# Kernel optimization log

Hardware: AMD Instinct MI355X
Metric: run time of the kernel (lower is better)

Reference implementation:

```python
import jax, jax.numpy as jnp
import numpy as np

T = 2048        # q_len (current chunk)
P = 2048        # past KV cache length
HID = 4096      # hidden_size
H = 32          # num_attention_heads
D = HID // H    # head_dim = 128
THETA = 10000.0


def apply_rope(x, pos):
    # x: [H, T, D], pos: [T] int
    half = D // 2
    inv_freq = 1.0 / (THETA ** (jnp.arange(0, half, dtype=jnp.float32) / half))
    ang = pos.astype(jnp.float32)[:, None] * inv_freq[None, :]      # [T, D/2]
    cos = jnp.concatenate([jnp.cos(ang), jnp.cos(ang)], axis=-1)[None]  # [1, T, D]
    sin = jnp.concatenate([jnp.sin(ang), jnp.sin(ang)], axis=-1)[None]
    rot = jnp.concatenate([-x[..., half:], x[..., :half]], axis=-1)
    return x * cos + rot * sin


def setup_inputs() -> dict:
    key = jax.random.key(0)
    ks = jax.random.split(key, 8)
    s = 1.0 / np.sqrt(HID)
    inp = {
        "hidden_states": jax.random.normal(ks[0], (T, HID), dtype=jnp.float32),
        "attention_mask": jnp.triu(jnp.full((T, T), -jnp.inf, dtype=jnp.float32), k=1),
        "Wq": jax.random.normal(ks[1], (HID, HID), dtype=jnp.float32) * s,
        "Wk": jax.random.normal(ks[2], (HID, HID), dtype=jnp.float32) * s,
        "Wv": jax.random.normal(ks[3], (HID, HID), dtype=jnp.float32) * s,
        "Wo": jax.random.normal(ks[4], (HID, HID), dtype=jnp.float32) * s,
        "past_k": jax.random.normal(ks[5], (H, P, D), dtype=jnp.float32),
        "past_v": jax.random.normal(ks[6], (H, P, D), dtype=jnp.float32),
        "position_ids": P + jnp.arange(T, dtype=jnp.int32),
        "past_length": P,
    }
    return inp


def reference(hidden_states, attention_mask, Wq, Wk, Wv, Wo, past_k, past_v,
              position_ids, past_length):
    # QKV projections -> [H, T, D]
    proj = lambda W: (hidden_states @ W).reshape(T, H, D).transpose(1, 0, 2)
    q, k, v = proj(Wq), proj(Wk), proj(Wv)
    q = apply_rope(q, position_ids)
    k = apply_rope(k, position_ids)

    scale = 1.0 / jnp.sqrt(jnp.float32(D))
    # scores against past cache and current chunk (fp32 softmax, as in source)
    past_dots = (jnp.einsum('htd,hsd->hts', q, past_k) * scale).astype(jnp.float32)
    pmask = jnp.where(jnp.arange(P) < past_length, 0.0, -jnp.inf)  # [P]
    past_dots = past_dots + pmask
    cur = ((jnp.einsum('htd,hsd->hts', q, k) * scale) + attention_mask).astype(jnp.float32)

    # online-softmax merge via logsumexp combination
    past_lse = jax.scipy.special.logsumexp(past_dots, axis=-1, keepdims=True)
    cur_lse = jax.scipy.special.logsumexp(cur, axis=-1, keepdims=True)
    tot_lse = jnp.logaddexp(past_lse, cur_lse)
    pw = jnp.exp(past_dots - tot_lse).astype(q.dtype)
    cw = jnp.exp(cur - tot_lse).astype(q.dtype)

    out = jnp.einsum('hts,hsd->htd', pw, past_v) + jnp.einsum('hts,hsd->htd', cw, v)
    out = jnp.where(past_length == 0,
                    jnp.einsum('hts,hsd->htd', jax.nn.softmax(cur, axis=-1).astype(q.dtype), v),
                    out)
    out = out.transpose(1, 0, 2).reshape(T, HID)   # [T, hidden]
    return out @ Wo
```

## Files before the change

kernel.cpp:

```cpp
#include <hip/hip_runtime.h>
#include <cstdint>
#include <cstddef>

#define T_LEN 2048
#define PAST_MAX 2048
#define HID 4096
#define NHEAD 32
#define DHEAD 128

typedef __bf16 bf16_t;
typedef __bf16 bf16x4 __attribute__((ext_vector_type(4)));
typedef __bf16 bf16x8 __attribute__((ext_vector_type(8)));
typedef float  f32x4  __attribute__((ext_vector_type(4)));
typedef float  f32x16 __attribute__((ext_vector_type(16)));
typedef unsigned int u32x4 __attribute__((ext_vector_type(4)));

__device__ __forceinline__ void gload16(const void* g, void* l){
  __builtin_amdgcn_global_load_lds((const __attribute__((address_space(1))) void*)g,
                                   (__attribute__((address_space(3))) void*)l,
                                   16, 0, 0);
}

__device__ __forceinline__ unsigned pack_bf16(float a, float b){
  const unsigned ua = __builtin_bit_cast(unsigned short, (bf16_t)a);
  const unsigned ub = __builtin_bit_cast(unsigned short, (bf16_t)b);
  return ua | (ub << 16);
}

__global__ void cvt2_k(const float* __restrict__ a, bf16_t* __restrict__ ao,
                       const float* __restrict__ b, bf16_t* __restrict__ bo, int n4){
  int i = blockIdx.x * 256 + threadIdx.x;
  if (i < n4){
    const float4 v = ((const float4*)a)[i];
    bf16x4 o = { (bf16_t)v.x, (bf16_t)v.y, (bf16_t)v.z, (bf16_t)v.w };
    ((bf16x4*)ao)[i] = o;
  } else {
    i -= n4;
    const float4 v = ((const float4*)b)[i];
    bf16x4 o = { (bf16_t)v.x, (bf16_t)v.y, (bf16_t)v.z, (bf16_t)v.w };
    ((bf16x4*)bo)[i] = o;
  }
}

__global__ __launch_bounds__(256) void transpose2_k(const float* __restrict__ in,
                                                    bf16_t* __restrict__ out, int R, int C){
  __shared__ float tile[64][65];
  const int r0 = blockIdx.x << 6, c0 = blockIdx.y << 6;
  const size_t bo = (size_t)blockIdx.z * (size_t)R * (size_t)C;
  const int tx = threadIdx.x & 15, ty = threadIdx.x >> 4;
#pragma unroll
  for (int k = 0; k < 4; ++k){
    const float4 v = *(const float4*)(in + bo + (size_t)(r0 + ty + 16*k) * C + c0 + tx*4);
    float* tp = &tile[ty + 16*k][tx*4];
    tp[0] = v.x; tp[1] = v.y; tp[2] = v.z; tp[3] = v.w;
  }
  __syncthreads();
  const int rr0 = (threadIdx.x & 7) * 8;
  const int ccb = threadIdx.x >> 3;
#pragma unroll
  for (int k = 0; k < 2; ++k){
    const int cc = ccb + 32*k;
    bf16x8 o;
#pragma unroll
    for (int j = 0; j < 8; ++j) o[j] = (bf16_t)tile[rr0 + j][cc];
    *(bf16x8*)(out + bo + (size_t)(c0 + cc) * R + r0 + rr0) = o;
  }
}

__global__ __launch_bounds__(256) void transpose3_k(
    const float* __restrict__ s0, const float* __restrict__ s1, const float* __restrict__ s2,
    bf16_t* __restrict__ d0, bf16_t* __restrict__ d1, bf16_t* __restrict__ d2){
  __shared__ float tile[64][65];
  const float* in = (blockIdx.z == 0) ? s0 : (blockIdx.z == 1) ? s1 : s2;
  bf16_t* out = (blockIdx.z == 0) ? d0 : (blockIdx.z == 1) ? d1 : d2;
  const int r0 = blockIdx.x << 6, c0 = blockIdx.y << 6;
  const int tx = threadIdx.x & 15, ty = threadIdx.x >> 4;
#pragma unroll
  for (int k = 0; k < 4; ++k){
    const float4 v = *(const float4*)(in + (size_t)(r0 + ty + 16*k) * HID + c0 + tx*4);
    float* tp = &tile[ty + 16*k][tx*4];
    tp[0] = v.x; tp[1] = v.y; tp[2] = v.z; tp[3] = v.w;
  }
  __syncthreads();
  const int rr0 = (threadIdx.x & 7) * 8;
  const int ccb = threadIdx.x >> 3;
#pragma unroll
  for (int k = 0; k < 2; ++k){
    const int cc = ccb + 32*k;
    bf16x8 o;
#pragma unroll
    for (int j = 0; j < 8; ++j) o[j] = (bf16_t)tile[rr0 + j][cc];
    *(bf16x8*)(out + (size_t)(c0 + cc) * HID + r0 + rr0) = o;
  }
}

__global__ void ropek_k(bf16_t* __restrict__ K, const int* __restrict__ pos){
  const int idx = blockIdx.x * 256 + threadIdx.x;
  const int i = idx & 63;
  const int t = (idx >> 6) & (T_LEN - 1);
  const int h = idx >> 17;
  const size_t base = ((size_t)h * T_LEN + t) * DHEAD;
  const float p = (float)pos[t];
  const float inv = __expf(-(float)i * 0.14391156605212898f);
  const float ang = p * inv;
  float sn, cs;
  sincosf(ang, &sn, &cs);
  const float b0 = (float)K[base + i], b1 = (float)K[base + i + 64];
  K[base + i]      = (bf16_t)(b0 * cs - b1 * sn);
  K[base + i + 64] = (bf16_t)(b1 * cs + b0 * sn);
}

__global__ __launch_bounds__(512, 2) void gemm2b_k(
    const bf16_t* __restrict__ A,
    const bf16_t* __restrict__ B0, const bf16_t* __restrict__ B1, const bf16_t* __restrict__ B2,
    bf16_t* __restrict__ OQ, bf16_t* __restrict__ OK2, bf16_t* __restrict__ OVT, int cpx)
{
  const int bid = blockIdx.x;
  const int wg  = (bid & 7) * cpx + (bid >> 3);
  const int mt  = wg & 7;
  const int rest = wg >> 3;
  const int z   = rest >> 5;
  const int nt  = rest & 31;
  const int m0  = mt << 8;
  const int n0  = nt << 7;
  const bf16_t* __restrict__ B = (z == 0) ? B0 : (z == 1) ? B1 : B2;

  const int tid = threadIdx.x;
  const int wv = tid >> 6, lane = tid & 63, lm = lane & 15, g = lane >> 4;
  const int wr = wv >> 1, wc = wv & 1;

  __shared__ __align__(16) char smem[49152];

  const f32x4 fzero = {0.f, 0.f, 0.f, 0.f};
  f32x4 acc[4][4];
#pragma unroll
  for (int i = 0; i < 4; ++i)
#pragma unroll
    for (int j = 0; j < 4; ++j) acc[i][j] = fzero;

  size_t aoff[2], boff;
#pragma unroll
  for (int i = 0; i < 2; ++i){
    const int c = i * 512 + tid;
    const int row = c >> 2, gr = c & 3;
    const int srcg = gr ^ ((row >> 1) & 3);
    aoff[i] = (size_t)(m0 + row) * HID + srcg * 8;
  }
  {
    const int row = tid >> 2, gr = tid & 3;
    const int srcg = gr ^ ((row >> 1) & 3);
    boff = (size_t)(n0 + row) * HID + srcg * 8;
  }
  const int adst0 = ((0 * 512 + wv * 64) << 4);
  const int adst1 = ((1 * 512 + wv * 64) << 4);
  const int bdst  = ((wv * 64) << 4);

  auto stage = [&](int kt){
    char* ab = smem + (kt & 1) * 24576;
    char* bb = ab + 16384;
    const bf16_t* Ak = A + kt * 32;
    const bf16_t* Bk = B + kt * 32;
    gload16(Ak + aoff[0], ab + adst0);
    gload16(Ak + aoff[1], ab + adst1);
    gload16(Bk + boff,    bb + bdst);
  };

  const int ksw = ((g ^ ((lm >> 1) & 3)) << 4);
  const int arow = (wr * 64 + lm) * 64;
  const int brow = (wc * 64 + lm) * 64;

  const int NT = HID / 32;
  stage(0);
  for (int t = 0; t < NT; ++t){
    if (t + 1 < NT){
      stage(t + 1);
      asm volatile("s_waitcnt vmcnt(3)" ::: "memory");
    } else {
      asm volatile("s_waitcnt vmcnt(0)" ::: "memory");
    }
    __builtin_amdgcn_s_barrier();

    char* ab = smem + (t & 1) * 24576;
    char* bb = ab + 16384;
    bf16x8 af[4], bfv[4];
#pragma unroll
    for (int mf = 0; mf < 4; ++mf)
      af[mf] = *(const bf16x8*)(ab + arow + mf * 1024 + ksw);
#pragma unroll
    for (int ni = 0; ni < 4; ++ni)
      bfv[ni] = *(const bf16x8*)(bb + brow + ni * 1024 + ksw);
    __builtin_amdgcn_s_setprio(1);
#pragma unroll
    for (int mf = 0; mf < 4; ++mf)
#pragma unroll
      for (int ni = 0; ni < 4; ++ni)
        acc[mf][ni] = __builtin_amdgcn_mfma_f32_16x16x32_bf16(af[mf], bfv[ni], acc[mf][ni], 0, 0, 0);
    __builtin_amdgcn_s_setprio(0);
    __builtin_amdgcn_s_barrier();
  }

#pragma unroll
  for (int ni = 0; ni < 4; ++ni){
    const int col = n0 + wc * 64 + ni * 16 + lm;
    const int hh = col >> 7, dd = col & 127;
#pragma unroll
    for (int mf = 0; mf < 4; ++mf)
#pragma unroll
      for (int r = 0; r < 4; ++r){
        const int trow = m0 + wr * 64 + mf * 16 + g * 4 + r;
        const bf16_t v = (bf16_t)acc[mf][ni][r];
        if (z == 2)      OVT[((size_t)hh * DHEAD + dd) * T_LEN + trow] = v;
        else if (z == 1) OK2[((size_t)hh * T_LEN + trow) * DHEAD + dd] = v;
        else             OQ [((size_t)hh * T_LEN + trow) * DHEAD + dd] = v;
      }
  }
}

__global__ __launch_bounds__(512, 1) void gemm4p_k(
    const bf16_t* __restrict__ A, const bf16_t* __restrict__ B,
    float* __restrict__ OF, int cpx)
{
  const int bid = blockIdx.x;
  const int wg  = (bid & 7) * cpx + (bid >> 3);
  const int mt  = wg & 7;
  const int nt  = wg >> 3;
  const int m0  = mt << 8;
  const int n0  = nt << 7;

  const int tid = threadIdx.x;
  const int wv = tid >> 6, lane = tid & 63, lm = lane & 15, g = lane >> 4;
  const int wr = wv >> 1, wc = wv & 1;

  __shared__ __align__(16) char smem[98304];

  const f32x4 fzero = {0.f, 0.f, 0.f, 0.f};
  f32x4 acc[4][4];
#pragma unroll
  for (int i = 0; i < 4; ++i)
#pragma unroll
    for (int j = 0; j < 4; ++j) acc[i][j] = fzero;

  int srow[2], schk[2];
#pragma unroll
  for (int i = 0; i < 2; ++i){
    const int c = i * 512 + tid;
    srow[i] = c >> 3;
    schk[i] = (c & 7) ^ (srow[i] & 7);
  }
  const int sdst0 = ((0 * 512 + wv * 64) << 4);
  const int sdst1 = ((1 * 512 + wv * 64) << 4);

  auto stg = [&](int kt, int op){
    if (kt < 64){
      char* dst = smem + (kt & 1) * 49152 + op * 16384;
      const bf16_t* base = (op < 2) ? A + (size_t)(m0 + (op << 7)) * HID
                                    : B + (size_t)n0 * HID;
      base += kt * 64;
      gload16(base + (size_t)srow[0] * HID + schk[0] * 8, dst + sdst0);
      gload16(base + (size_t)srow[1] * HID + schk[1] * 8, dst + sdst1);
    }
  };

  const int koff0 = ((g)     ^ (lm & 7)) << 4;
  const int koff1 = ((4 + g) ^ (lm & 7)) << 4;
  const int abase = ((wr >> 1) << 14) + ((((wr & 1) << 6) + lm) << 7);
  const int bbase = 32768 + ((((wc << 6)) + lm) << 7);

  bf16x8 bfr[4][2];
  auto dsB = [&](int buf){
    const char* p = smem + buf * 49152 + bbase;
#pragma unroll
    for (int ni = 0; ni < 4; ++ni){
      bfr[ni][0] = *(const bf16x8*)(p + ni * 2048 + koff0);
      bfr[ni][1] = *(const bf16x8*)(p + ni * 2048 + koff1);
    }
  };

  stg(0, 2);
  stg(0, 0); stg(0, 1);
  stg(1, 2);
  asm volatile("s_waitcnt vmcnt(2)" ::: "memory");
  __builtin_amdgcn_s_barrier();

  for (int t = 0; t < 32; ++t){
    const int c0 = 2 * t, c1 = 2 * t + 1;
    const bool last = (t == 31);

#pragma unroll
    for (int half = 0; half < 2; ++half){
      const char* bufp = smem + half * 49152;
      bf16x8 afr[2][2];
      dsB(half);
#pragma unroll
      for (int mf = 0; mf < 2; ++mf){
        afr[mf][0] = *(const bf16x8*)(bufp + abase + mf * 2048 + koff0);
        afr[mf][1] = *(const bf16x8*)(bufp + abase + mf * 2048 + koff1);
      }
      if (half == 0){ stg(c1, 0); stg(c1, 1); }
      else          { stg(c0 + 2, 0); stg(c0 + 2, 1); }
      __builtin_amdgcn_s_barrier();
      asm volatile("s_waitcnt lgkmcnt(0)" ::: "memory");
      __builtin_amdgcn_s_setprio(1);
#pragma unroll
      for (int kk = 0; kk < 2; ++kk)
#pragma unroll
        for (int mf = 0; mf < 2; ++mf)
#pragma unroll
          for (int ni = 0; ni < 4; ++ni)
            acc[mf][ni] = __builtin_amdgcn_mfma_f32_16x16x32_bf16(afr[mf][kk], bfr[ni][kk], acc[mf][ni], 0, 0, 0);
      __builtin_amdgcn_s_setprio(0);
      __builtin_amdgcn_s_barrier();

#pragma unroll
      for (int mf = 0; mf < 2; ++mf){
        afr[mf][0] = *(const bf16x8*)(bufp + abase + (mf + 2) * 2048 + koff0);
        afr[mf][1] = *(const bf16x8*)(bufp + abase + (mf + 2) * 2048 + koff1);
      }
      if (half == 0) stg(c0 + 2, 2);
      else           stg(c1 + 2, 2);
      if (last) asm volatile("s_waitcnt vmcnt(0)" ::: "memory");
      else      asm volatile("s_waitcnt vmcnt(2)" ::: "memory");
      __builtin_amdgcn_s_barrier();
      asm volatile("s_waitcnt lgkmcnt(0)" ::: "memory");
      __builtin_amdgcn_s_setprio(1);
#pragma unroll
      for (int kk = 0; kk < 2; ++kk)
#pragma unroll
        for (int mf = 0; mf < 2; ++mf)
#pragma unroll
          for (int ni = 0; ni < 4; ++ni)
            acc[mf + 2][ni] = __builtin_amdgcn_mfma_f32_16x16x32_bf16(afr[mf][kk], bfr[ni][kk], acc[mf + 2][ni], 0, 0, 0);
      __builtin_amdgcn_s_setprio(0);
      __builtin_amdgcn_s_barrier();
    }
  }

#pragma unroll
  for (int ni = 0; ni < 4; ++ni){
    const int col = n0 + wc * 64 + ni * 16 + lm;
#pragma unroll
    for (int mf = 0; mf < 4; ++mf)
#pragma unroll
      for (int r = 0; r < 4; ++r){
        const int trow = m0 + wr * 64 + mf * 16 + g * 4 + r;
        OF[(size_t)trow * HID + col] = acc[mf][ni][r];
      }
  }
}

__global__ __launch_bounds__(256, 2) void attn2_k(
    const bf16_t* __restrict__ Q,
    const bf16_t* __restrict__ Kc,
    const bf16_t* __restrict__ VTc,
    const bf16_t* __restrict__ Kp,
    const bf16_t* __restrict__ VTp,
    bf16_t* __restrict__ Ctx,
    const int* __restrict__ plen_p,
    const int* __restrict__ pos)
{
  const int bid = blockIdx.x;
  const int xcd = bid & 7;
  const int k   = bid >> 3;
  const int ho  = k >> 4;
  const int qraw= k & 15;
  const int h   = (xcd << 2) | ho;
  const int qb  = (ho & 2) ? (15 - qraw) : qraw;

  const int tid = threadIdx.x;
  const int w = tid >> 6, lane = tid & 63, l31 = lane & 31, hi = lane >> 5;
  const int qw0 = qb * 128 + w * 32;
  const int qrow = qw0 + l31;
  const int plen = plen_p[0];
  const int npast = (plen + 63) >> 6;
  const int NT = npast + 2 * qb + 2;

  __shared__ __align__(16) char smem[65536 + 512];
  float* lred = (float*)(smem + 65536);

  const bf16_t* qbase = Q + ((size_t)h * T_LEN + qrow) * DHEAD;
  bf16x8 qf[8];
#pragma unroll
  for (int dc = 0; dc < 8; ++dc)
    qf[dc] = *(const bf16x8*)(qbase + dc * 16 + 8 * hi);
  {
    const float ppos = (float)pos[qrow];
    const float qs = 0.08838834764831845f;
#pragma unroll
    for (int dc = 0; dc < 4; ++dc)
#pragma unroll
      for (int j = 0; j < 8; ++j){
        const int fi = dc * 16 + 8 * hi + j;
        const float invf = __expf(-(float)fi * 0.14391156605212898f);
        float sn, cs;
        sincosf(ppos * invf, &sn, &cs);
        const float a0 = (float)qf[dc][j], a1 = (float)qf[dc + 4][j];
        qf[dc][j]     = (bf16_t)((a0 * cs - a1 * sn) * qs);
        qf[dc + 4][j] = (bf16_t)((a1 * cs + a0 * sn) * qs);
      }
  }
  __builtin_amdgcn_sched_barrier(0);

  const f32x16 fz = {0.f,0.f,0.f,0.f,0.f,0.f,0.f,0.f,0.f,0.f,0.f,0.f,0.f,0.f,0.f,0.f};
  f32x16 o[4] = {fz, fz, fz, fz};
  float m = -1e30f, l = 0.f;

  auto stage = [&](int t, int buf){
    const bf16_t* kb; const bf16_t* vb;
    if (t < npast){
      const int s0 = t * 64;
      kb = Kp  + ((size_t)h * PAST_MAX + s0) * DHEAD;
      vb = VTp + (size_t)h * DHEAD * PAST_MAX + s0;
    } else {
      const int s0 = (t - npast) * 64;
      kb = Kc  + ((size_t)h * T_LEN + s0) * DHEAD;
      vb = VTc + (size_t)h * DHEAD * T_LEN + s0;
    }
    char* kl = smem + buf * 32768;
    char* vl = kl + 16384;
#pragma unroll
    for (int i = 0; i < 4; ++i){
      const int c = i * 256 + w * 64 + lane;
      const int krow = c >> 4, kcol = c & 15;
      gload16(kb + (size_t)krow * DHEAD + ((kcol ^ (krow & 7)) << 3), kl + (i * 256 + w * 64) * 16);
      const int vrow = c >> 3, vcol = c & 7;
      gload16(vb + (size_t)vrow * 2048 + ((vcol ^ (vrow & 7)) << 3), vl + (i * 256 + w * 64) * 16);
    }
  };

  stage(0, 0);
  __builtin_amdgcn_sched_barrier(0);

  for (int t = 0; t < NT; ++t){
    const int cur = t & 1;
    if (t + 1 < NT){
      stage(t + 1, cur ^ 1);
      asm volatile("s_waitcnt vmcnt(8)" ::: "memory");
    } else {
      asm volatile("s_waitcnt vmcnt(0)" ::: "memory");
    }
    __builtin_amdgcn_sched_barrier(0);
    __builtin_amdgcn_s_barrier();
    __builtin_amdgcn_sched_barrier(0);

    const bool isc = (t >= npast);
    const int s0c = (t - npast) * 64;
    const bool active = !isc || (s0c <= qw0 + 31);

    if (active){
      char* kl = smem + cur * 32768;
      char* vl = kl + 16384;

      f32x16 sacc[2] = {fz, fz};
      __builtin_amdgcn_s_setprio(1);
#pragma unroll
      for (int kvh = 0; kvh < 2; ++kvh){
        const int krow = (kvh << 5) + l31;
        const int kbo = krow << 8;
        const int sw = (krow & 7) << 4;
#pragma unroll
        for (int dc = 0; dc < 8; ++dc){
          const bf16x8 kf = *(const bf16x8*)(kl + kbo + ((dc * 32 + 16 * hi) ^ sw));
          sacc[kvh] = __builtin_amdgcn_mfma_f32_32x32x16_bf16(kf, qf[dc], sacc[kvh], 0, 0, 0);
        }
      }
      __builtin_amdgcn_s_setprio(0);

      const bool mcur  = isc && (s0c + 63 > qw0);
      const bool mpast = !isc && ((t + 1) * 64 > plen);
      float pv[2][16];
      float pm = -1e30f;
      if (mcur | mpast){
#pragma unroll
        for (int kvh = 0; kvh < 2; ++kvh)
#pragma unroll
          for (int r = 0; r < 16; ++r){
            float x = sacc[kvh][r];
            const int kvoff = (kvh << 5) + (r & 3) + 8 * (r >> 2) + 4 * hi;
            if (mcur  && (s0c + kvoff >  qrow)) x = -1e30f;
            if (mpast && (t * 64 + kvoff >= plen)) x = -1e30f;
            pv[kvh][r] = x;
            pm = fmaxf(pm, x);
          }
      } else {
#pragma unroll
        for (int kvh = 0; kvh < 2; ++kvh)
#pragma unroll
          for (int r = 0; r < 16; ++r){
            pv[kvh][r] = sacc[kvh][r];
            pm = fmaxf(pm, sacc[kvh][r]);
          }
      }
      pm = fmaxf(pm, __shfl_xor(pm, 32));

      if (!__all(pm - m <= 8.f)){
        const float mn = fmaxf(m, pm);
        const float corr = __expf(m - mn);
        m = mn;
        l *= corr;
        if (hi == 0) lred[(w << 5) + l31] = corr;
        asm volatile("s_waitcnt lgkmcnt(0)" ::: "memory");
#pragma unroll
        for (int r = 0; r < 16; ++r){
          const float cc = lred[(w << 5) + (r & 3) + 8 * (r >> 2) + 4 * hi];
#pragma unroll
          for (int nb = 0; nb < 4; ++nb) o[nb][r] *= cc;
        }
      }

      float sum = 0.f;
#pragma unroll
      for (int kvh = 0; kvh < 2; ++kvh)
#pragma unroll
        for (int r = 0; r < 16; ++r){
          const float pe = __expf(pv[kvh][r] - m);
          pv[kvh][r] = pe;
          sum += pe;
        }
      sum += __shfl_xor(sum, 32);
      l += sum;

      unsigned wds[2][8];
#pragma unroll
      for (int kvh = 0; kvh < 2; ++kvh)
#pragma unroll
        for (int i = 0; i < 8; ++i)
          wds[kvh][i] = pack_bf16(pv[kvh][2 * i], pv[kvh][2 * i + 1]);

      bf16x8 pf[4];
#pragma unroll
      for (int ks = 0; ks < 4; ++ks){
        const int s = ks & 1, kvh = ks >> 1;
        const unsigned a0 = hi ? wds[kvh][4 * s]     : wds[kvh][4 * s + 2];
        const unsigned a1 = hi ? wds[kvh][4 * s + 1] : wds[kvh][4 * s + 3];
        const unsigned z0 = (unsigned)__shfl_xor((int)a0, 32);
        const unsigned z1 = (unsigned)__shfl_xor((int)a1, 32);
        u32x4 fw;
        fw[0] = hi ? z0 : wds[kvh][4 * s];
        fw[1] = hi ? z1 : wds[kvh][4 * s + 1];
        fw[2] = hi ? wds[kvh][4 * s + 2] : z0;
        fw[3] = hi ? wds[kvh][4 * s + 3] : z1;
        pf[ks] = __builtin_bit_cast(bf16x8, fw);
      }

      __builtin_amdgcn_s_setprio(1);
#pragma unroll
      for (int ks = 0; ks < 4; ++ks)
#pragma unroll
        for (int nb = 0; nb < 4; ++nb){
          const int vrow = (nb << 5) + l31;
          const bf16x8 vf = *(const bf16x8*)(vl + (vrow << 7) + ((ks * 32 + 16 * hi) ^ ((vrow & 7) << 4)));
          o[nb] = __builtin_amdgcn_mfma_f32_32x32x16_bf16(pf[ks], vf, o[nb], 0, 0, 0);
        }
      __builtin_amdgcn_s_setprio(0);
    }
    __builtin_amdgcn_sched_barrier(0);
    __builtin_amdgcn_s_barrier();
  }

  if (hi == 0) lred[(w << 5) + l31] = l;
  asm volatile("s_waitcnt lgkmcnt(0)" ::: "memory");
#pragma unroll
  for (int r = 0; r < 16; ++r){
    const int cr = (r & 3) + 8 * (r >> 2) + 4 * hi;
    const float li = 1.f / lred[(w << 5) + cr];
    const int trow = qw0 + cr;
    bf16_t* cb = Ctx + (size_t)trow * HID + h * DHEAD + l31;
#pragma unroll
    for (int nb = 0; nb < 4; ++nb)
      cb[nb << 5] = (bf16_t)(o[nb][r] * li);
  }
}

extern "C" void kernel_launch(void* const* d_in, const int* in_sizes, int n_in,
                              void* d_out, int out_size, void* d_ws, size_t ws_size,
                              hipStream_t stream)
{
  const float* X   = (const float*)d_in[0];
  const float* Wq  = (const float*)d_in[2];
  const float* Wk  = (const float*)d_in[3];
  const float* Wv  = (const float*)d_in[4];
  const float* Wo  = (const float*)d_in[5];
  const float* PKi = (const float*)d_in[6];
  const float* PVi = (const float*)d_in[7];
  const int* POS   = (const int*)d_in[8];
  const int* PLEN  = (const int*)d_in[9];
  float* OUT = (float*)d_out;

  char* ws = (char*)d_ws;
  const size_t SZ_XB  = (size_t)T_LEN * HID * 2;
  const size_t SZ_W   = (size_t)HID * HID * 2;
  const size_t SZ_HTD = (size_t)NHEAD * T_LEN * DHEAD * 2;

  bf16_t* XB  = (bf16_t*)(ws);
  bf16_t* WT0 = (bf16_t*)(ws + SZ_XB);
  bf16_t* WT1 = (bf16_t*)(ws + SZ_XB + SZ_W);
  bf16_t* WT2 = (bf16_t*)(ws + SZ_XB + 2 * SZ_W);
  char* p = ws + SZ_XB + 3 * SZ_W;
  bf16_t* QB   = (bf16_t*)p; p += SZ_HTD;
  bf16_t* KB   = (bf16_t*)p; p += SZ_HTD;
  bf16_t* VTB  = (bf16_t*)p; p += SZ_HTD;
  bf16_t* KPB  = (bf16_t*)p; p += SZ_HTD;
  bf16_t* VPTB = (bf16_t*)p; p += SZ_HTD;
  bf16_t* CTX  = (bf16_t*)p; p += SZ_HTD;
  bf16_t* WOT  = QB;

  dim3 blk256(256);
  dim3 blk512(512);
  cvt2_k<<<16384, blk256, 0, stream>>>(X, XB, PKi, KPB, T_LEN * HID / 4);
  transpose3_k<<<dim3(64,64,3), blk256, 0, stream>>>(Wq, Wk, Wv, WT0, WT1, WT2);
  transpose2_k<<<dim3(32,2,32), blk256, 0, stream>>>(PVi, VPTB, PAST_MAX, DHEAD);

  gemm2b_k<<<768, blk512, 0, stream>>>(XB, WT0, WT1, WT2, QB, KB, VTB, 96);
  ropek_k<<<16384, blk256, 0, stream>>>(KB, POS);
  attn2_k<<<512, blk256, 0, stream>>>(QB, KB, VTB, KPB, VPTB, CTX, PLEN, POS);

  transpose2_k<<<dim3(64,64,1), blk256, 0, stream>>>(Wo, WOT, HID, HID);
  gemm4p_k<<<256, blk512, 0, stream>>>(CTX, WOT, OUT, 32);
}
```

Measured before the change: 584.2 us.

## Restructure QKV GEMM main loop into deeper split-stage pipeline with K=64 tiles

The QKV projection GEMM's main loop is rewritten. K-tiles grow from 32 to 64 columns, LDS doubles to 96KB, and the XOR swizzle now works over 8 chunks. Each K step is split into two halves: global loads for the next A and B tiles are issued partway through, and the MFMAs run on half of the M fragments at a time, so transfers overlap compute at finer granularity. Launch bounds drop to one block per CU, trading occupancy for larger tiles and fewer barriers per unit of K.

Result: no change. 582.4 us (-0.3%).

```diff
diff --git a/kernel.cpp b/kernel.cpp
--- a/kernel.cpp
+++ b/kernel.cpp
@@ -110,7 +110,7 @@
   K[base + i + 64] = (bf16_t)(b1 * cs + b0 * sn);
 }
 
-__global__ __launch_bounds__(512, 2) void gemm2b_k(
+__global__ __launch_bounds__(512, 1) void gemmqkv4p_k(
     const bf16_t* __restrict__ A,
     const bf16_t* __restrict__ B0, const bf16_t* __restrict__ B1, const bf16_t* __restrict__ B2,
     bf16_t* __restrict__ OQ, bf16_t* __restrict__ OK2, bf16_t* __restrict__ OVT, int cpx)
@@ -129,7 +129,7 @@
   const int wv = tid >> 6, lane = tid & 63, lm = lane & 15, g = lane >> 4;
   const int wr = wv >> 1, wc = wv & 1;
 
-  __shared__ __align__(16) char smem[49152];
+  __shared__ __align__(16) char smem[98304];
 
   const f32x4 fzero = {0.f, 0.f, 0.f, 0.f};
   f32x4 acc[4][4];
@@ -138,65 +138,99 @@
 #pragma unroll
     for (int j = 0; j < 4; ++j) acc[i][j] = fzero;
 
-  size_t aoff[2], boff;
+  int srow[2], schk[2];
 #pragma unroll
   for (int i = 0; i < 2; ++i){
     const int c = i * 512 + tid;
-    const int row = c >> 2, gr = c & 3;
-    const int srcg = gr ^ ((row >> 1) & 3);
-    aoff[i] = (size_t)(m0 + row) * HID + srcg * 8;
-  }
-  {
-    const int row = tid >> 2, gr = tid & 3;
-    const int srcg = gr ^ ((row >> 1) & 3);
-    boff = (size_t)(n0 + row) * HID + srcg * 8;
-  }
-  const int adst0 = ((0 * 512 + wv * 64) << 4);
-  const int adst1 = ((1 * 512 + wv * 64) << 4);
-  const int bdst  = ((wv * 64) << 4);
-
-  auto stage = [&](int kt){
-    char* ab = smem + (kt & 1) * 24576;
-    char* bb = ab + 16384;
-    const bf16_t* Ak = A + kt * 32;
-    const bf16_t* Bk = B + kt * 32;
-    gload16(Ak + aoff[0], ab + adst0);
-    gload16(Ak + aoff[1], ab + adst1);
-    gload16(Bk + boff,    bb + bdst);
+    srow[i] = c >> 3;
+    schk[i] = (c & 7) ^ (srow[i] & 7);
+  }
+  const int sdst0 = ((0 * 512 + wv * 64) << 4);
+  const int sdst1 = ((1 * 512 + wv * 64) << 4);
+
+  auto stg = [&](int kt, int op){
+    if (kt < 64){
+      char* dst = smem + (kt & 1) * 49152 + op * 16384;
+      const bf16_t* base = (op < 2) ? A + (size_t)(m0 + (op << 7)) * HID
+                                    : B + (size_t)n0 * HID;
+      base += kt * 64;
+      gload16(base + (size_t)srow[0] * HID + schk[0] * 8, dst + sdst0);
+      gload16(base + (size_t)srow[1] * HID + schk[1] * 8, dst + sdst1);
+    }
   };
 
-  const int ksw = ((g ^ ((lm >> 1) & 3)) << 4);
-  const int arow = (wr * 64 + lm) * 64;
-  const int brow = (wc * 64 + lm) * 64;
-
-  const int NT = HID / 32;
-  stage(0);
-  for (int t = 0; t < NT; ++t){
-    if (t + 1 < NT){
-      stage(t + 1);
-      asm volatile("s_waitcnt vmcnt(3)" ::: "memory");
-    } else {
-      asm volatile("s_waitcnt vmcnt(0)" ::: "memory");
-    }
-    __builtin_amdgcn_s_barrier();
-
-    char* ab = smem + (t & 1) * 24576;
-    char* bb = ab + 16384;
-    bf16x8 af[4], bfv[4];
-#pragma unroll
-    for (int mf = 0; mf < 4; ++mf)
-      af[mf] = *(const bf16x8*)(ab + arow + mf * 1024 + ksw);
-#pragma unroll
-    for (int ni = 0; ni < 4; ++ni)
-      bfv[ni] = *(const bf16x8*)(bb + brow + ni * 1024 + ksw);
-    __builtin_amdgcn_s_setprio(1);
-#pragma unroll
-    for (int mf = 0; mf < 4; ++mf)
-#pragma unroll
-      for (int ni = 0; ni < 4; ++ni)
-        acc[mf][ni] = __builtin_amdgcn_mfma_f32_16x16x32_bf16(af[mf], bfv[ni], acc[mf][ni], 0, 0, 0);
-    __builtin_amdgcn_s_setprio(0);
-    __builtin_amdgcn_s_barrier();
+  const int koff0 = ((g)     ^ (lm & 7)) << 4;
+  const int koff1 = ((4 + g) ^ (lm & 7)) << 4;
+  const int abase = ((wr >> 1) << 14) + ((((wr & 1) << 6) + lm) << 7);
+  const int bbase = 32768 + ((((wc << 6)) + lm) << 7);
+
+  bf16x8 bfr[4][2];
+  auto dsB = [&](int buf){
+    const char* p = smem + buf * 49152 + bbase;
+#pragma unroll
+    for (int ni = 0; ni < 4; ++ni){
+      bfr[ni][0] = *(const bf16x8*)(p + ni * 2048 + koff0);
+      bfr[ni][1] = *(const bf16x8*)(p + ni * 2048 + koff1);
+    }
+  };
+
+  stg(0, 2);
+  stg(0, 0); stg(0, 1);
+  stg(1, 2);
+  asm volatile("s_waitcnt vmcnt(2)" ::: "memory");
+  __builtin_amdgcn_s_barrier();
+
+  for (int t = 0; t < 32; ++t){
+    const int c0 = 2 * t, c1 = 2 * t + 1;
+    const bool last = (t == 31);
+
+#pragma unroll
+    for (int half = 0; half < 2; ++half){
+      const char* bufp = smem + half * 49152;
+      bf16x8 afr[2][2];
+      dsB(half);
+#pragma unroll
+      for (int mf = 0; mf < 2; ++mf){
+        afr[mf][0] = *(const bf16x8*)(bufp + abase + mf * 2048 + koff0);
+        afr[mf][1] = *(const bf16x8*)(bufp + abase + mf * 2048 + koff1);
+      }
+      if (half == 0){ stg(c1, 0); stg(c1, 1); }
+      else          { stg(c0 + 2, 0); stg(c0 + 2, 1); }
+      __builtin_amdgcn_s_barrier();
+      asm volatile("s_waitcnt lgkmcnt(0)" ::: "memory");
+      __builtin_amdgcn_s_setprio(1);
+#pragma unroll
+      for (int kk = 0; kk < 2; ++kk)
+#pragma unroll
+        for (int mf = 0; mf < 2; ++mf)
+#pragma unroll
+          for (int ni = 0; ni < 4; ++ni)
+            acc[mf][ni] = __builtin_amdgcn_mfma_f32_16x16x32_bf16(afr[mf][kk], bfr[ni][kk], acc[mf][ni], 0, 0, 0);
+      __builtin_amdgcn_s_setprio(0);
+      __builtin_amdgcn_s_barrier();
+
+#pragma unroll
+      for (int mf = 0; mf < 2; ++mf){
+        afr[mf][0] = *(const bf16x8*)(bufp + abase + (mf + 2) * 2048 + koff0);
+        afr[mf][1] = *(const bf16x8*)(bufp + abase + (mf + 2) * 2048 + koff1);
+      }
+      if (half == 0) stg(c0 + 2, 2);
+      else           stg(c1 + 2, 2);
+      if (last) asm volatile("s_waitcnt vmcnt(0)" ::: "memory");
+      else      asm volatile("s_waitcnt vmcnt(2)" ::: "memory");
+      __builtin_amdgcn_s_barrier();
+      asm volatile("s_waitcnt lgkmcnt(0)" ::: "memory");
+      __builtin_amdgcn_s_setprio(1);
+#pragma unroll
+      for (int kk = 0; kk < 2; ++kk)
+#pragma unroll
+        for (int mf = 0; mf < 2; ++mf)
+#pragma unroll
+          for (int ni = 0; ni < 4; ++ni)
+            acc[mf + 2][ni] = __builtin_amdgcn_mfma_f32_16x16x32_bf16(afr[mf][kk], bfr[ni][kk], acc[mf + 2][ni], 0, 0, 0);
+      __builtin_amdgcn_s_setprio(0);
+      __builtin_amdgcn_s_barrier();
+    }
   }
 
 #pragma unroll
@@ -610,7 +644,7 @@
   transpose3_k<<<dim3(64,64,3), blk256, 0, stream>>>(Wq, Wk, Wv, WT0, WT1, WT2);
   transpose2_k<<<dim3(32,2,32), blk256, 0, stream>>>(PVi, VPTB, PAST_MAX, DHEAD);
 
-  gemm2b_k<<<768, blk512, 0, stream>>>(XB, WT0, WT1, WT2, QB, KB, VTB, 96);
+  gemmqkv4p_k<<<768, blk512, 0, stream>>>(XB, WT0, WT1, WT2, QB, KB, VTB, 96);
   ropek_k<<<16384, blk256, 0, stream>>>(KB, POS);
   attn2_k<<<512, blk256, 0, stream>>>(QB, KB, VTB, KPB, VPTB, CTX, PLEN, POS);
 
```

## Use four-stage LDS ring with register double-buffering in both projection GEMMs

Applied to the files above, without the earlier changes.

Both the QKV and output-projection GEMMs now use a 4-slot LDS ring (BK=32) with loads issued three stages ahead and LDS fragment reads ping-ponged between two register sets, so MFMAs on one stage overlap the reads of the next. The output GEMM drops its split-half BK=64 scheme for this unified schedule. The QKV GEMM doubles its shared memory to 96KB and lowers launch bounds to one block per CU, trading occupancy for deeper prefetch.

New measurement: 596.5 us. 1.02x slower.

```diff
diff --git a/kernel.cpp b/kernel.cpp
--- a/kernel.cpp
+++ b/kernel.cpp
@@ -110,7 +110,7 @@
   K[base + i + 64] = (bf16_t)(b1 * cs + b0 * sn);
 }
 
-__global__ __launch_bounds__(512, 2) void gemm2b_k(
+__global__ __launch_bounds__(512, 1) void gemmqkv_rr_k(
     const bf16_t* __restrict__ A,
     const bf16_t* __restrict__ B0, const bf16_t* __restrict__ B1, const bf16_t* __restrict__ B2,
     bf16_t* __restrict__ OQ, bf16_t* __restrict__ OK2, bf16_t* __restrict__ OVT, int cpx)
@@ -129,7 +129,7 @@
   const int wv = tid >> 6, lane = tid & 63, lm = lane & 15, g = lane >> 4;
   const int wr = wv >> 1, wc = wv & 1;
 
-  __shared__ __align__(16) char smem[49152];
+  __shared__ __align__(16) char smem[98304];
 
   const f32x4 fzero = {0.f, 0.f, 0.f, 0.f};
   f32x4 acc[4][4];
@@ -155,40 +155,34 @@
   const int adst1 = ((1 * 512 + wv * 64) << 4);
   const int bdst  = ((wv * 64) << 4);
 
-  auto stage = [&](int kt){
-    char* ab = smem + (kt & 1) * 24576;
-    char* bb = ab + 16384;
-    const bf16_t* Ak = A + kt * 32;
-    const bf16_t* Bk = B + kt * 32;
-    gload16(Ak + aoff[0], ab + adst0);
-    gload16(Ak + aoff[1], ab + adst1);
-    gload16(Bk + boff,    bb + bdst);
+  auto stg = [&](int kt){
+    if (kt < 128){
+      char* ab = smem + (kt & 3) * 24576;
+      char* bb = ab + 16384;
+      const bf16_t* Ak = A + kt * 32;
+      const bf16_t* Bk = B + kt * 32;
+      gload16(Ak + aoff[0], ab + adst0);
+      gload16(Ak + aoff[1], ab + adst1);
+      gload16(Bk + boff,    bb + bdst);
+    }
   };
 
   const int ksw = ((g ^ ((lm >> 1) & 3)) << 4);
   const int arow = (wr * 64 + lm) * 64;
   const int brow = (wc * 64 + lm) * 64;
 
-  const int NT = HID / 32;
-  stage(0);
-  for (int t = 0; t < NT; ++t){
-    if (t + 1 < NT){
-      stage(t + 1);
-      asm volatile("s_waitcnt vmcnt(3)" ::: "memory");
-    } else {
-      asm volatile("s_waitcnt vmcnt(0)" ::: "memory");
-    }
-    __builtin_amdgcn_s_barrier();
-
-    char* ab = smem + (t & 1) * 24576;
-    char* bb = ab + 16384;
-    bf16x8 af[4], bfv[4];
+  auto rd = [&](int kt, bf16x8 (&af)[4], bf16x8 (&bfv)[4]){
+    const char* ab = smem + (kt & 3) * 24576;
+    const char* bb = ab + 16384;
 #pragma unroll
     for (int mf = 0; mf < 4; ++mf)
       af[mf] = *(const bf16x8*)(ab + arow + mf * 1024 + ksw);
 #pragma unroll
     for (int ni = 0; ni < 4; ++ni)
       bfv[ni] = *(const bf16x8*)(bb + brow + ni * 1024 + ksw);
+  };
+
+  auto mm = [&](bf16x8 (&af)[4], bf16x8 (&bfv)[4]){
     __builtin_amdgcn_s_setprio(1);
 #pragma unroll
     for (int mf = 0; mf < 4; ++mf)
@@ -196,7 +190,32 @@
       for (int ni = 0; ni < 4; ++ni)
         acc[mf][ni] = __builtin_amdgcn_mfma_f32_16x16x32_bf16(af[mf], bfv[ni], acc[mf][ni], 0, 0, 0);
     __builtin_amdgcn_s_setprio(0);
+  };
+
+  bf16x8 afA[4], bfA[4], afB[4], bfB[4];
+  stg(0); stg(1); stg(2);
+  asm volatile("s_waitcnt vmcnt(6)" ::: "memory");
+  __builtin_amdgcn_s_barrier();
+  rd(0, afA, bfA);
+
+  for (int i = 0; i < 64; ++i){
+    const int e = 2 * i;
+    if (e <= 125) asm volatile("s_waitcnt vmcnt(3)" ::: "memory");
+    else          asm volatile("s_waitcnt vmcnt(0)" ::: "memory");
     __builtin_amdgcn_s_barrier();
+    rd(e + 1, afB, bfB);
+    stg(e + 3);
+    __builtin_amdgcn_sched_barrier(0);
+    mm(afA, bfA);
+
+    const int o = e + 1;
+    if (o <= 125) asm volatile("s_waitcnt vmcnt(3)" ::: "memory");
+    else          asm volatile("s_waitcnt vmcnt(0)" ::: "memory");
+    __builtin_amdgcn_s_barrier();
+    if (o < 127) rd(o + 1, afA, bfA);
+    stg(o + 3);
+    __builtin_amdgcn_sched_barrier(0);
+    mm(afB, bfB);
   }
 
 #pragma unroll
@@ -216,7 +235,7 @@
   }
 }
 
-__global__ __launch_bounds__(512, 1) void gemm4p_k(
+__global__ __launch_bounds__(512, 1) void gemmop_rr_k(
     const bf16_t* __restrict__ A, const bf16_t* __restrict__ B,
     float* __restrict__ OF, int cpx)
 {
@@ -240,99 +259,84 @@
 #pragma unroll
     for (int j = 0; j < 4; ++j) acc[i][j] = fzero;
 
-  int srow[2], schk[2];
+  size_t aoff[2], boff;
 #pragma unroll
   for (int i = 0; i < 2; ++i){
     const int c = i * 512 + tid;
-    srow[i] = c >> 3;
-    schk[i] = (c & 7) ^ (srow[i] & 7);
-  }
-  const int sdst0 = ((0 * 512 + wv * 64) << 4);
-  const int sdst1 = ((1 * 512 + wv * 64) << 4);
-
-  auto stg = [&](int kt, int op){
-    if (kt < 64){
-      char* dst = smem + (kt & 1) * 49152 + op * 16384;
-      const bf16_t* base = (op < 2) ? A + (size_t)(m0 + (op << 7)) * HID
-                                    : B + (size_t)n0 * HID;
-      base += kt * 64;
-      gload16(base + (size_t)srow[0] * HID + schk[0] * 8, dst + sdst0);
-      gload16(base + (size_t)srow[1] * HID + schk[1] * 8, dst + sdst1);
+    const int row = c >> 2, gr = c & 3;
+    const int srcg = gr ^ ((row >> 1) & 3);
+    aoff[i] = (size_t)(m0 + row) * HID + srcg * 8;
+  }
+  {
+    const int row = tid >> 2, gr = tid & 3;
+    const int srcg = gr ^ ((row >> 1) & 3);
+    boff = (size_t)(n0 + row) * HID + srcg * 8;
+  }
+  const int adst0 = ((0 * 512 + wv * 64) << 4);
+  const int adst1 = ((1 * 512 + wv * 64) << 4);
+  const int bdst  = ((wv * 64) << 4);
+
+  auto stg = [&](int kt){
+    if (kt < 128){
+      char* ab = smem + (kt & 3) * 24576;
+      char* bb = ab + 16384;
+      const bf16_t* Ak = A + kt * 32;
+      const bf16_t* Bk = B + kt * 32;
+      gload16(Ak + aoff[0], ab + adst0);
+      gload16(Ak + aoff[1], ab + adst1);
+      gload16(Bk + boff,    bb + bdst);
     }
   };
 
-  const int koff0 = ((g)     ^ (lm & 7)) << 4;
-  const int koff1 = ((4 + g) ^ (lm & 7)) << 4;
-  const int abase = ((wr >> 1) << 14) + ((((wr & 1) << 6) + lm) << 7);
-  const int bbase = 32768 + ((((wc << 6)) + lm) << 7);
-
-  bf16x8 bfr[4][2];
-  auto dsB = [&](int buf){
-    const char* p = smem + buf * 49152 + bbase;
-#pragma unroll
-    for (int ni = 0; ni < 4; ++ni){
-      bfr[ni][0] = *(const bf16x8*)(p + ni * 2048 + koff0);
-      bfr[ni][1] = *(const bf16x8*)(p + ni * 2048 + koff1);
-    }
+  const int ksw = ((g ^ ((lm >> 1) & 3)) << 4);
+  const int arow = (wr * 64 + lm) * 64;
+  const int brow = (wc * 64 + lm) * 64;
+
+  auto rd = [&](int kt, bf16x8 (&af)[4], bf16x8 (&bfv)[4]){
+    const char* ab = smem + (kt & 3) * 24576;
+    const char* bb = ab + 16384;
+#pragma unroll
+    for (int mf = 0; mf < 4; ++mf)
+      af[mf] = *(const bf16x8*)(ab + arow + mf * 1024 + ksw);
+#pragma unroll
+    for (int ni = 0; ni < 4; ++ni)
+      bfv[ni] = *(const bf16x8*)(bb + brow + ni * 1024 + ksw);
   };
 
-  stg(0, 2);
-  stg(0, 0); stg(0, 1);
-  stg(1, 2);
-  asm volatile("s_waitcnt vmcnt(2)" ::: "memory");
+  auto mm = [&](bf16x8 (&af)[4], bf16x8 (&bfv)[4]){
+    __builtin_amdgcn_s_setprio(1);
+#pragma unroll
+    for (int mf = 0; mf < 4; ++mf)
+#pragma unroll
+      for (int ni = 0; ni < 4; ++ni)
+        acc[mf][ni] = __builtin_amdgcn_mfma_f32_16x16x32_bf16(af[mf], bfv[ni], acc[mf][ni], 0, 0, 0);
+    __builtin_amdgcn_s_setprio(0);
+  };
+
+  bf16x8 afA[4], bfA[4], afB[4], bfB[4];
+  stg(0); stg(1); stg(2);
+  asm volatile("s_waitcnt vmcnt(6)" ::: "memory");
   __builtin_amdgcn_s_barrier();
-
-  for (int t = 0; t < 32; ++t){
-    const int c0 = 2 * t, c1 = 2 * t + 1;
-    const bool last = (t == 31);
-
-#pragma unroll
-    for (int half = 0; half < 2; ++half){
-      const char* bufp = smem + half * 49152;
-      bf16x8 afr[2][2];
-      dsB(half);
-#pragma unroll
-      for (int mf = 0; mf < 2; ++mf){
-        afr[mf][0] = *(const bf16x8*)(bufp + abase + mf * 2048 + koff0);
-        afr[mf][1] = *(const bf16x8*)(bufp + abase + mf * 2048 + koff1);
-      }
-      if (half == 0){ stg(c1, 0); stg(c1, 1); }
-      else          { stg(c0 + 2, 0); stg(c0 + 2, 1); }
-      __builtin_amdgcn_s_barrier();
-      asm volatile("s_waitcnt lgkmcnt(0)" ::: "memory");
-      __builtin_amdgcn_s_setprio(1);
-#pragma unroll
-      for (int kk = 0; kk < 2; ++kk)
-#pragma unroll
-        for (int mf = 0; mf < 2; ++mf)
-#pragma unroll
-          for (int ni = 0; ni < 4; ++ni)
-            acc[mf][ni] = __builtin_amdgcn_mfma_f32_16x16x32_bf16(afr[mf][kk], bfr[ni][kk], acc[mf][ni], 0, 0, 0);
-      __builtin_amdgcn_s_setprio(0);
-      __builtin_amdgcn_s_barrier();
-
-#pragma unroll
-      for (int mf = 0; mf < 2; ++mf){
-        afr[mf][0] = *(const bf16x8*)(bufp + abase + (mf + 2) * 2048 + koff0);
-        afr[mf][1] = *(const bf16x8*)(bufp + abase + (mf + 2) * 2048 + koff1);
-      }
-      if (half == 0) stg(c0 + 2, 2);
-      else           stg(c1 + 2, 2);
-      if (last) asm volatile("s_waitcnt vmcnt(0)" ::: "memory");
-      else      asm volatile("s_waitcnt vmcnt(2)" ::: "memory");
-      __builtin_amdgcn_s_barrier();
-      asm volatile("s_waitcnt lgkmcnt(0)" ::: "memory");
-      __builtin_amdgcn_s_setprio(1);
-#pragma unroll
-      for (int kk = 0; kk < 2; ++kk)
-#pragma unroll
-        for (int mf = 0; mf < 2; ++mf)
-#pragma unroll
-          for (int ni = 0; ni < 4; ++ni)
-            acc[mf + 2][ni] = __builtin_amdgcn_mfma_f32_16x16x32_bf16(afr[mf][kk], bfr[ni][kk], acc[mf + 2][ni], 0, 0, 0);
-      __builtin_amdgcn_s_setprio(0);
-      __builtin_amdgcn_s_barrier();
-    }
+  rd(0, afA, bfA);
+
+  for (int i = 0; i < 64; ++i){
+    const int e = 2 * i;
+    if (e <= 125) asm volatile("s_waitcnt vmcnt(3)" ::: "memory");
+    else          asm volatile("s_waitcnt vmcnt(0)" ::: "memory");
+    __builtin_amdgcn_s_barrier();
+    rd(e + 1, afB, bfB);
+    stg(e + 3);
+    __builtin_amdgcn_sched_barrier(0);
+    mm(afA, bfA);
+
+    const int o = e + 1;
+    if (o <= 125) asm volatile("s_waitcnt vmcnt(3)" ::: "memory");
+    else          asm volatile("s_waitcnt vmcnt(0)" ::: "memory");
+    __builtin_amdgcn_s_barrier();
+    if (o < 127) rd(o + 1, afA, bfA);
+    stg(o + 3);
+    __builtin_amdgcn_sched_barrier(0);
+    mm(afB, bfB);
   }
 
 #pragma unroll
@@ -610,10 +614,10 @@
   transpose3_k<<<dim3(64,64,3), blk256, 0, stream>>>(Wq, Wk, Wv, WT0, WT1, WT2);
   transpose2_k<<<dim3(32,2,32), blk256, 0, stream>>>(PVi, VPTB, PAST_MAX, DHEAD);
 
-  gemm2b_k<<<768, blk512, 0, stream>>>(XB, WT0, WT1, WT2, QB, KB, VTB, 96);
+  gemmqkv_rr_k<<<768, blk512, 0, stream>>>(XB, WT0, WT1, WT2, QB, KB, VTB, 96);
   ropek_k<<<16384, blk256, 0, stream>>>(KB, POS);
   attn2_k<<<512, blk256, 0, stream>>>(QB, KB, VTB, KPB, VPTB, CTX, PLEN, POS);
 
   transpose2_k<<<dim3(64,64,1), blk256, 0, stream>>>(Wo, WOT, HID, HID);
-  gemm4p_k<<<256, blk512, 0, stream>>>(CTX, WOT, OUT, 32);
-}
+  gemmop_rr_k<<<256, blk512, 0, stream>>>(CTX, WOT, OUT, 32);
+}
```
